# Kernel tuning notes

Measured on AMD Instinct MI355X. Metric: run time of the kernel, lower is better.

The kernel has to match this reference:

```python
import jax, jax.numpy as jnp
import numpy as np
from jax import lax

DN = ('NCHW', 'OIHW', 'NCHW')


def setup_inputs() -> dict:
    key = jax.random.key(0)
    ks = jax.random.split(key, 7)
    B, IC, OC, H, W = 8, 64, 64, 128, 128
    return {
        'x': jax.random.normal(ks[0], (B, IC, H, W), jnp.float32),
        'w3': jax.random.normal(ks[1], (OC, IC, 3, 3), jnp.float32) * 0.05,
        'b3': jax.random.normal(ks[2], (OC,), jnp.float32) * 0.05,
        'w5': jax.random.normal(ks[3], (OC, IC, 5, 5), jnp.float32) * 0.05,
        'b5': jax.random.normal(ks[4], (OC,), jnp.float32) * 0.05,
        'wr': jax.random.normal(ks[5], (OC, 10, 1, 1), jnp.float32) * 0.1,
        'br': jax.random.normal(ks[6], (OC,), jnp.float32) * 0.05,
    }


def reference(x, w3, b3, w5, b5, wr, br):
    # Two 'same' convs (k=3 pad 1, k=5 pad 2) as in layers['5']
    y3 = lax.conv_general_dilated(x, w3, (1, 1), 'SAME', dimension_numbers=DN) + b3[None, :, None, None]
    y5 = lax.conv_general_dilated(x, w5, (1, 1), 'SAME', dimension_numbers=DN) + b5[None, :, None, None]
    B, C, H, W = y3.shape
    # The nested pad/crop loop == 9 zero-padded unit shifts of y3:
    # stackedFeatures order per channel: [y5, shift(sh=0,sw=0..2), shift(sh=1,...), ...]
    # shifted[h, w] = y3[h + 1 - sw, w + 1 - sh] with zero padding.
    P = jnp.pad(y3, ((0, 0), (0, 0), (1, 1), (1, 1)))
    shifts = [P[:, :, 2 - sw:2 - sw + H, 2 - sh:2 - sh + W]
              for sh in range(3) for sw in range(3)]
    stacked = jnp.stack([y5] + shifts, axis=2)  # [B, C, 10, H, W]
    # remap: grouped 1x1 conv, groups=OC, 10 in-channels per group
    out = jnp.einsum('bcghw,cg->bchw', stacked, wr[:, :, 0, 0]) + br[None, :, None, None]
    return out
```

## Files before the change

### kernel.cpp

```cpp
#include <hip/hip_runtime.h>

typedef unsigned short u16;
typedef unsigned int u32;
typedef __attribute__((ext_vector_type(8))) short short8;
typedef __attribute__((ext_vector_type(4))) short short4v;
typedef __attribute__((ext_vector_type(4))) float floatx4;

#define XP 72

__device__ __forceinline__ float bf2f(u16 u) {
    u32 b = ((u32)u) << 16;
    return __builtin_bit_cast(float, b);
}
__device__ __forceinline__ u16 f2bf(float f) {
    u32 b = __builtin_bit_cast(u32, f);
    b += 0x7FFFu + ((b >> 16) & 1u);
    return (u16)(b >> 16);
}

typedef __attribute__((address_space(3))) u16 lds_u16;
typedef const __attribute__((address_space(1))) u16 glob_u16;
__device__ __forceinline__ void gl_lds16(const u16* g, u16* l) {
    __builtin_amdgcn_global_load_lds((glob_u16*)g, (lds_u16*)l, 16, 0, 0);
}

__device__ __forceinline__ float load_any(const void* p, int i, int isf32) {
    return isf32 ? ((const float*)p)[i] : bf2f(((const u16*)p)[i]);
}

__device__ __forceinline__ int sniff_f(const void* x, int* scnt) {
    if (threadIdx.x == 0) *scnt = 0;
    __syncthreads();
    int c = 0;
#pragma unroll
    for (int k = 0; k < 8; ++k) {
        u16 u = ((const u16*)x)[2 * (threadIdx.x * 8 + k)];
        int e = (u >> 7) & 0xFF;
        if (e >= 140) c++;
    }
    if (c) atomicAdd(scnt, c);
    __syncthreads();
    return (*scnt >= 8) ? 1 : 0;
}

#define W5C_BYTE 0
#define SCAL_BYTE 204800
#define V_BYTE 207616
#define XT_BYTE 1272576
#define N_W5C 102400
#define N_SCAL 704
#define PACK_N2 (N_W5C + N_SCAL)

#define VIRT_BLKS 32
#define PACK_BLKS ((PACK_N2 + 255) / 256)
#define TRANS_BLKS 4096

__global__ __launch_bounds__(256) void fuse1(
        const void* __restrict__ x, const void* __restrict__ w3,
        const void* __restrict__ b3, const void* __restrict__ w5,
        const void* __restrict__ b5, const void* __restrict__ wr,
        const void* __restrict__ br,
        u16* __restrict__ w5c, float* __restrict__ scal,
        float* __restrict__ V, u16* __restrict__ xt) {
    __shared__ __align__(16) u16 smem[132 * XP];
    __shared__ int scnt;
    const int bid = blockIdx.x;
    const int tid = threadIdx.x;
    const int f = sniff_f(x, &scnt);

    if (bid < VIRT_BLKS) {
        const int side = bid & 3, b = bid >> 2;
        const int fixed = (side & 1) ? 127 : 0;
        {
            short8 z = {0, 0, 0, 0, 0, 0, 0, 0};
            short8* sp = (short8*)smem;
            for (int i = tid; i < (132 * XP) / 8; i += 256) sp[i] = z;
        }
        __syncthreads();
        {
            const int ic = tid & 63, g = tid >> 6;
            if (side < 2) {
                if (f) {
                    const float* xp = (const float*)x +
                        ((size_t)(b * 64 + ic) * 128 + fixed) * 128;
                    for (int c0 = g * 32; c0 < g * 32 + 32; c0 += 4) {
                        float4 v = *(const float4*)(xp + c0);
                        smem[(c0 + 2) * XP + ic] = f2bf(v.x);
                        smem[(c0 + 3) * XP + ic] = f2bf(v.y);
                        smem[(c0 + 4) * XP + ic] = f2bf(v.z);
                        smem[(c0 + 5) * XP + ic] = f2bf(v.w);
                    }
                } else {
                    const u16* xp = (const u16*)x +
                        ((size_t)(b * 64 + ic) * 128 + fixed) * 128;
                    for (int c0 = g * 32; c0 < g * 32 + 32; c0 += 8) {
                        short8 v = *(const short8*)(xp + c0);
#pragma unroll
                        for (int e = 0; e < 8; ++e)
                            smem[(c0 + 2 + e) * XP + ic] = (u16)v[e];
                    }
                }
            } else {
                if (f) {
                    const float* xp = (const float*)x +
                        (size_t)(b * 64 + ic) * 16384 + fixed;
                    for (int cc = g * 32; cc < g * 32 + 32; ++cc)
                        smem[(cc + 2) * XP + ic] = f2bf(xp[(size_t)cc * 128]);
                } else {
                    const u16* xp = (const u16*)x +
                        (size_t)(b * 64 + ic) * 16384 + fixed;
                    for (int cc = g * 32; cc < g * 32 + 32; ++cc)
                        smem[(cc + 2) * XP + ic] = xp[(size_t)cc * 128];
                }
            }
        }
        const int wv = tid >> 6, lane = tid & 63, cb = lane & 15, q = lane >> 4;
        const int oc = wv * 16 + cb;
        short8 aaA[6];
#pragma unroll
        for (int ks = 0; ks < 6; ++ks) {
            const int kbase = ks * 32 + q * 8;
            const int kk = kbase >> 6, ic0 = kbase & 63;
            int r, c;
            if (side == 0)      { r = 2;  c = kk; }
            else if (side == 1) { r = 0;  c = kk; }
            else if (side == 2) { r = kk; c = 2;  }
            else                { r = kk; c = 0;  }
            short8 a;
#pragma unroll
            for (int j = 0; j < 8; ++j)
                a[j] = (short)f2bf(load_any(w3, (oc * 64 + ic0 + j) * 9 + r * 3 + c, f));
            aaA[ks] = a;
        }
        __syncthreads();

        floatx4 acc[9];
#pragma unroll
        for (int nt = 0; nt < 9; ++nt) acc[nt] = (floatx4){0.f, 0.f, 0.f, 0.f};
#pragma unroll
        for (int ks = 0; ks < 6; ++ks) {
            const int kbase = ks * 32 + q * 8;
            const int kk = kbase >> 6, ic0 = kbase & 63;
#pragma unroll
            for (int nt = 0; nt < 9; ++nt) {
                int p = nt * 16 + cb + kk;
                if (nt == 8 && p > 131) p = 131;
                short8 bb = *(const short8*)&smem[p * XP + ic0];
                acc[nt] = __builtin_amdgcn_mfma_f32_16x16x32_bf16(aaA[ks], bb,
                                                                  acc[nt], 0, 0, 0);
            }
        }
#pragma unroll
        for (int nt = 0; nt < 9; ++nt) {
            int pos = nt * 16 + cb;
            if (pos < 130) {
#pragma unroll
                for (int reg = 0; reg < 4; ++reg) {
                    int oco = wv * 16 + q * 4 + reg;
                    V[((size_t)(b * 4 + side) * 130 + pos) * 64 + oco] =
                        acc[nt][reg] + load_any(b3, oco, f);
                }
            }
        }
        return;
    }

    if (bid < VIRT_BLKS + PACK_BLKS) {
        const int i = (bid - VIRT_BLKS) * 256 + tid;
        if (i >= PACK_N2) return;
        if (i < N_W5C) {
            int j = i & 7, lane = (i >> 3) & 63, mt = (i >> 9) & 3, ks = i >> 11;
            int oc = mt * 16 + (lane & 15);
            int k = ks * 32 + ((lane >> 4) & 3) * 8 + j;
            int tap = k >> 6, ic = k & 63;
            int kh = tap / 5, kw = tap - kh * 5;
            int dh = kh - 2, dw = kw - 2;
            float v = load_any(wr, oc * 10, f) * load_any(w5, (oc * 64 + ic) * 25 + tap, f);
            for (int sw = 0; sw < 3; ++sw) {
                int r = dh + sw;
                if (r < 0 || r > 2) continue;
                for (int sh = 0; sh < 3; ++sh) {
                    int c = dw + sh;
                    if (c < 0 || c > 2) continue;
                    v += load_any(wr, oc * 10 + 1 + sh * 3 + sw, f) *
                         load_any(w3, (oc * 64 + ic) * 9 + r * 3 + c, f);
                }
            }
            w5c[i] = f2bf(v);
        } else {
            int i2 = i - N_W5C;
            float v;
            if (i2 < 64) {
                int oc = i2;
                float swr = 0.f;
                for (int g = 1; g <= 9; ++g) swr += load_any(wr, oc * 10 + g, f);
                v = load_any(wr, oc * 10, f) * load_any(b5, oc, f) +
                    swr * load_any(b3, oc, f) + load_any(br, oc, f);
            } else {
                v = load_any(wr, i2 - 64, f);
            }
            scal[i2] = v;
        }
        return;
    }

    {
        const int t2 = bid - (VIRT_BLKS + PACK_BLKS);
        const int b = t2 >> 9, h = (t2 >> 2) & 127, w0 = (t2 & 3) * 32;
        const int t = tid;
        if (f) {
            const int w2 = t & 15, ic = t >> 4;
#pragma unroll
            for (int p = 0; p < 4; ++p) {
                int icc = ic + p * 16;
                const float* src = (const float*)x +
                    (((size_t)(b * 64 + icc) * 128 + h) * 128 + w0 + 2 * w2);
                float2 v = *(const float2*)src;
                smem[(2 * w2) * XP + icc]     = f2bf(v.x);
                smem[(2 * w2 + 1) * XP + icc] = f2bf(v.y);
            }
        } else {
            const int w4 = t & 7, ic = t >> 3;
#pragma unroll
            for (int p = 0; p < 2; ++p) {
                int icc = ic + p * 32;
                const u16* src = (const u16*)x +
                    (((size_t)(b * 64 + icc) * 128 + h) * 128 + w0 + 4 * w4);
                short4v v = *(const short4v*)src;
#pragma unroll
                for (int e = 0; e < 4; ++e)
                    smem[(4 * w4 + e) * XP + icc] = (u16)v[e];
            }
        }
        __syncthreads();
        const int w = t >> 3, qq = t & 7;
        short8 v = *(const short8*)&smem[w * XP + qq * 8];
        *(short8*)(xt + ((size_t)((b * 128 + h) * 128) + w0 + w) * 64 + qq * 8) = v;
    }
}

__device__ floatx4 edge_fix4(
        const float* __restrict__ Vb, const float* __restrict__ wrf,
        int gh, int gw, int oc0, floatx4 s) {
#pragma unroll
    for (int sh = 0; sh < 3; ++sh)
#pragma unroll
        for (int sw = 0; sw < 3; ++sw) {
            const int qh = gh + 1 - sw, qw = gw + 1 - sh;
            int sd, pos;
            if (qh == -1)       { sd = 0; pos = qw + 1; }
            else if (qh == 128) { sd = 1; pos = qw + 1; }
            else if (qw == -1)  { sd = 2; pos = qh + 1; }
            else if (qw == 128) { sd = 3; pos = qh + 1; }
            else continue;
            const float* vp = Vb + ((size_t)sd * 130 + pos) * 64 + oc0;
            const int wi = 1 + sh * 3 + sw;
#pragma unroll
            for (int r = 0; r < 4; ++r)
                s[r] -= wrf[(oc0 + r) * 10 + wi] * vp[r];
        }
    return s;
}

__global__ __launch_bounds__(256, 2) void conv_fused(
        const void* __restrict__ x,
        const u16* __restrict__ xt, const u16* __restrict__ w5c,
        const float* __restrict__ scal, const float* __restrict__ V,
        void* __restrict__ out) {
    __shared__ __align__(16) u16 xs[400 * XP];
    __shared__ __align__(16) u16 wbuf[2][2][2048];
    __shared__ int scnt;
    const int b = blockIdx.z, h0 = blockIdx.y * 16, w0 = blockIdx.x * 16;
    const int tid = threadIdx.x;
    const int wv = tid >> 6, lane = tid & 63;
    const int f = sniff_f(x, &scnt);

    {
        const int q8 = tid & 7, p0 = tid >> 3;
        for (int it = 0; it < 13; ++it) {
            int px = p0 + it * 32;
            if (px < 400) {
                int r = px / 20, c = px - r * 20;
                int gh = h0 + r - 2, gw = w0 + c - 2;
                short8 v = {0, 0, 0, 0, 0, 0, 0, 0};
                if ((unsigned)gh < 128u && (unsigned)gw < 128u)
                    v = *(const short8*)(xt +
                            ((size_t)((b * 128 + gh) * 128 + gw)) * 64 + q8 * 8);
                *(short8*)&xs[px * XP + q8 * 8] = v;
            }
        }
    }
    gl_lds16(w5c + 0 * 2048 + wv * 512 + lane * 8, &wbuf[0][0][wv * 512]);
    gl_lds16(w5c + 1 * 2048 + wv * 512 + lane * 8, &wbuf[0][1][wv * 512]);
    __syncthreads();

    const int cb = lane & 15, q = lane >> 4, wv4 = wv * 4;
    floatx4 acc[4][4];
#pragma unroll
    for (int mt = 0; mt < 4; ++mt)
#pragma unroll
        for (int nt = 0; nt < 4; ++nt)
            acc[mt][nt] = (floatx4){0.f, 0.f, 0.f, 0.f};

#pragma unroll 1
    for (int tap = 0; tap < 25; ++tap) {
        const int p = tap & 1;
        if (tap + 1 < 25) {
            gl_lds16(w5c + (size_t)((tap + 1) * 2 + 0) * 2048 + wv * 512 + lane * 8,
                     &wbuf[p ^ 1][0][wv * 512]);
            gl_lds16(w5c + (size_t)((tap + 1) * 2 + 1) * 2048 + wv * 512 + lane * 8,
                     &wbuf[p ^ 1][1][wv * 512]);
        }
        const int kh = tap / 5, kw = tap - kh * 5;
#pragma unroll
        for (int s = 0; s < 2; ++s) {
            short8 aa[4], bb[4];
#pragma unroll
            for (int mt = 0; mt < 4; ++mt)
                aa[mt] = *(const short8*)&wbuf[p][s][mt * 512 + lane * 8];
#pragma unroll
            for (int nt = 0; nt < 4; ++nt)
                bb[nt] = *(const short8*)&xs[((wv4 + nt + kh) * 20 + cb + kw) * XP +
                                             s * 32 + q * 8];
#pragma unroll
            for (int nt = 0; nt < 4; ++nt)
#pragma unroll
                for (int mt = 0; mt < 4; ++mt)
                    acc[mt][nt] = __builtin_amdgcn_mfma_f32_16x16x32_bf16(
                        aa[mt], bb[nt], acc[mt][nt], 0, 0, 0);
        }
        __syncthreads();
    }

    const float* biasC = scal;
    const float* wrf = scal + 64;
    const float* Vb = V + (size_t)b * 4 * 130 * 64;
#pragma unroll
    for (int mt = 0; mt < 4; ++mt)
#pragma unroll
        for (int nt = 0; nt < 4; ++nt) {
            const int gh = h0 + wv4 + nt;
            const int gw = w0 + cb;
            const int oc0 = mt * 16 + q * 4;
            floatx4 s;
#pragma unroll
            for (int reg = 0; reg < 4; ++reg)
                s[reg] = acc[mt][nt][reg] + biasC[oc0 + reg];
            if (gh == 0 || gh == 127 || gw == 0 || gw == 127)
                s = edge_fix4(Vb, wrf, gh, gw, oc0, s);
#pragma unroll
            for (int reg = 0; reg < 4; ++reg) {
                size_t oidx = ((size_t)(b * 64 + oc0 + reg) * 128 + gh) * 128 + gw;
                if (f) ((float*)out)[oidx] = s[reg];
                else   ((u16*)out)[oidx]   = f2bf(s[reg]);
            }
        }
}

extern "C" void kernel_launch(void* const* d_in, const int* in_sizes, int n_in,
                              void* d_out, int out_size, void* d_ws, size_t ws_size,
                              hipStream_t stream) {
    const void* x  = d_in[0];
    const void* w3 = d_in[1];
    const void* b3 = d_in[2];
    const void* w5 = d_in[3];
    const void* b5 = d_in[4];
    const void* wr = d_in[5];
    const void* br = d_in[6];

    u16*   w5c  = (u16*)((char*)d_ws + W5C_BYTE);
    float* scal = (float*)((char*)d_ws + SCAL_BYTE);
    float* V    = (float*)((char*)d_ws + V_BYTE);
    u16*   xt   = (u16*)((char*)d_ws + XT_BYTE);

    fuse1<<<VIRT_BLKS + PACK_BLKS + TRANS_BLKS, 256, 0, stream>>>(
        x, w3, b3, w5, b5, wr, br, w5c, scal, V, xt);
    conv_fused<<<dim3(8, 8, 8), 256, 0, stream>>>(x, xt, w5c, scal, V, d_out);
}
```

Before: 166.5 us.

## Split fused prep kernel into sniff, pack/transpose, virtual-edge, and conv launches

Moves the dtype sniff into its own one-block kernel that writes a flag to workspace, so the other blocks read one int instead of each redoing the atomic sniff and its two barriers. The edge-correction (virtual y3 border) MFMA work becomes a separate kernel that reads the already-transposed bf16 xt rather than strided raw x columns. This removes per-block sniff overhead and the uncoalesced column gathers, but adds two extra kernel launches and serialises the edge work after the transpose.

```diff
diff --git a/kernel.cpp b/kernel.cpp
--- a/kernel.cpp
+++ b/kernel.cpp
@@ -28,145 +28,49 @@
     return isf32 ? ((const float*)p)[i] : bf2f(((const u16*)p)[i]);
 }
 
-__device__ __forceinline__ int sniff_f(const void* x, int* scnt) {
-    if (threadIdx.x == 0) *scnt = 0;
-    __syncthreads();
-    int c = 0;
-#pragma unroll
-    for (int k = 0; k < 8; ++k) {
-        u16 u = ((const u16*)x)[2 * (threadIdx.x * 8 + k)];
-        int e = (u >> 7) & 0xFF;
-        if (e >= 140) c++;
-    }
-    if (c) atomicAdd(scnt, c);
-    __syncthreads();
-    return (*scnt >= 8) ? 1 : 0;
-}
-
-#define W5C_BYTE 0
-#define SCAL_BYTE 204800
-#define V_BYTE 207616
-#define XT_BYTE 1272576
+#define FLAG_BYTE 0
+#define W5C_BYTE 256
+#define SCAL_BYTE 205056
+#define V_BYTE 207872
+#define XT_BYTE 1272832
 #define N_W5C 102400
 #define N_SCAL 704
 #define PACK_N2 (N_W5C + N_SCAL)
 
-#define VIRT_BLKS 32
 #define PACK_BLKS ((PACK_N2 + 255) / 256)
 #define TRANS_BLKS 4096
 
-__global__ __launch_bounds__(256) void fuse1(
+__global__ __launch_bounds__(256) void sniff_kernel(const u16* __restrict__ xu,
+                                                    int* __restrict__ flag) {
+    __shared__ int cnt;
+    if (threadIdx.x == 0) cnt = 0;
+    __syncthreads();
+    int c = 0;
+    for (int k = 0; k < 8; ++k) {
+        int idx = 2 * (threadIdx.x * 8 + k);
+        u16 u = xu[idx];
+        int e = (u >> 7) & 0xFF;
+        if (e >= 140) c++;
+    }
+    atomicAdd(&cnt, c);
+    __syncthreads();
+    if (threadIdx.x == 0) *flag = (cnt >= 8) ? 1 : 0;
+}
+
+__global__ __launch_bounds__(256) void pack_trans(
         const void* __restrict__ x, const void* __restrict__ w3,
         const void* __restrict__ b3, const void* __restrict__ w5,
         const void* __restrict__ b5, const void* __restrict__ wr,
-        const void* __restrict__ br,
+        const void* __restrict__ br, const int* __restrict__ flag,
         u16* __restrict__ w5c, float* __restrict__ scal,
-        float* __restrict__ V, u16* __restrict__ xt) {
-    __shared__ __align__(16) u16 smem[132 * XP];
-    __shared__ int scnt;
+        u16* __restrict__ xt) {
+    __shared__ u16 tbuf[32 * XP];
     const int bid = blockIdx.x;
     const int tid = threadIdx.x;
-    const int f = sniff_f(x, &scnt);
-
-    if (bid < VIRT_BLKS) {
-        const int side = bid & 3, b = bid >> 2;
-        const int fixed = (side & 1) ? 127 : 0;
-        {
-            short8 z = {0, 0, 0, 0, 0, 0, 0, 0};
-            short8* sp = (short8*)smem;
-            for (int i = tid; i < (132 * XP) / 8; i += 256) sp[i] = z;
-        }
-        __syncthreads();
-        {
-            const int ic = tid & 63, g = tid >> 6;
-            if (side < 2) {
-                if (f) {
-                    const float* xp = (const float*)x +
-                        ((size_t)(b * 64 + ic) * 128 + fixed) * 128;
-                    for (int c0 = g * 32; c0 < g * 32 + 32; c0 += 4) {
-                        float4 v = *(const float4*)(xp + c0);
-                        smem[(c0 + 2) * XP + ic] = f2bf(v.x);
-                        smem[(c0 + 3) * XP + ic] = f2bf(v.y);
-                        smem[(c0 + 4) * XP + ic] = f2bf(v.z);
-                        smem[(c0 + 5) * XP + ic] = f2bf(v.w);
-                    }
-                } else {
-                    const u16* xp = (const u16*)x +
-                        ((size_t)(b * 64 + ic) * 128 + fixed) * 128;
-                    for (int c0 = g * 32; c0 < g * 32 + 32; c0 += 8) {
-                        short8 v = *(const short8*)(xp + c0);
-#pragma unroll
-                        for (int e = 0; e < 8; ++e)
-                            smem[(c0 + 2 + e) * XP + ic] = (u16)v[e];
-                    }
-                }
-            } else {
-                if (f) {
-                    const float* xp = (const float*)x +
-                        (size_t)(b * 64 + ic) * 16384 + fixed;
-                    for (int cc = g * 32; cc < g * 32 + 32; ++cc)
-                        smem[(cc + 2) * XP + ic] = f2bf(xp[(size_t)cc * 128]);
-                } else {
-                    const u16* xp = (const u16*)x +
-                        (size_t)(b * 64 + ic) * 16384 + fixed;
-                    for (int cc = g * 32; cc < g * 32 + 32; ++cc)
-                        smem[(cc + 2) * XP + ic] = xp[(size_t)cc * 128];
-                }
-            }
-        }
-        const int wv = tid >> 6, lane = tid & 63, cb = lane & 15, q = lane >> 4;
-        const int oc = wv * 16 + cb;
-        short8 aaA[6];
-#pragma unroll
-        for (int ks = 0; ks < 6; ++ks) {
-            const int kbase = ks * 32 + q * 8;
-            const int kk = kbase >> 6, ic0 = kbase & 63;
-            int r, c;
-            if (side == 0)      { r = 2;  c = kk; }
-            else if (side == 1) { r = 0;  c = kk; }
-            else if (side == 2) { r = kk; c = 2;  }
-            else                { r = kk; c = 0;  }
-            short8 a;
-#pragma unroll
-            for (int j = 0; j < 8; ++j)
-                a[j] = (short)f2bf(load_any(w3, (oc * 64 + ic0 + j) * 9 + r * 3 + c, f));
-            aaA[ks] = a;
-        }
-        __syncthreads();
-
-        floatx4 acc[9];
-#pragma unroll
-        for (int nt = 0; nt < 9; ++nt) acc[nt] = (floatx4){0.f, 0.f, 0.f, 0.f};
-#pragma unroll
-        for (int ks = 0; ks < 6; ++ks) {
-            const int kbase = ks * 32 + q * 8;
-            const int kk = kbase >> 6, ic0 = kbase & 63;
-#pragma unroll
-            for (int nt = 0; nt < 9; ++nt) {
-                int p = nt * 16 + cb + kk;
-                if (nt == 8 && p > 131) p = 131;
-                short8 bb = *(const short8*)&smem[p * XP + ic0];
-                acc[nt] = __builtin_amdgcn_mfma_f32_16x16x32_bf16(aaA[ks], bb,
-                                                                  acc[nt], 0, 0, 0);
-            }
-        }
-#pragma unroll
-        for (int nt = 0; nt < 9; ++nt) {
-            int pos = nt * 16 + cb;
-            if (pos < 130) {
-#pragma unroll
-                for (int reg = 0; reg < 4; ++reg) {
-                    int oco = wv * 16 + q * 4 + reg;
-                    V[((size_t)(b * 4 + side) * 130 + pos) * 64 + oco] =
-                        acc[nt][reg] + load_any(b3, oco, f);
-                }
-            }
-        }
-        return;
-    }
-
-    if (bid < VIRT_BLKS + PACK_BLKS) {
-        const int i = (bid - VIRT_BLKS) * 256 + tid;
+    const int f = *flag;
+
+    if (bid < PACK_BLKS) {
+        const int i = bid * 256 + tid;
         if (i >= PACK_N2) return;
         if (i < N_W5C) {
             int j = i & 7, lane = (i >> 3) & 63, mt = (i >> 9) & 3, ks = i >> 11;
@@ -205,7 +109,7 @@
     }
 
     {
-        const int t2 = bid - (VIRT_BLKS + PACK_BLKS);
+        const int t2 = bid - PACK_BLKS;
         const int b = t2 >> 9, h = (t2 >> 2) & 127, w0 = (t2 & 3) * 32;
         const int t = tid;
         if (f) {
@@ -216,8 +120,8 @@
                 const float* src = (const float*)x +
                     (((size_t)(b * 64 + icc) * 128 + h) * 128 + w0 + 2 * w2);
                 float2 v = *(const float2*)src;
-                smem[(2 * w2) * XP + icc]     = f2bf(v.x);
-                smem[(2 * w2 + 1) * XP + icc] = f2bf(v.y);
+                tbuf[(2 * w2) * XP + icc]     = f2bf(v.x);
+                tbuf[(2 * w2 + 1) * XP + icc] = f2bf(v.y);
             }
         } else {
             const int w4 = t & 7, ic = t >> 3;
@@ -229,13 +133,90 @@
                 short4v v = *(const short4v*)src;
 #pragma unroll
                 for (int e = 0; e < 4; ++e)
-                    smem[(4 * w4 + e) * XP + icc] = (u16)v[e];
+                    tbuf[(4 * w4 + e) * XP + icc] = (u16)v[e];
             }
         }
         __syncthreads();
         const int w = t >> 3, qq = t & 7;
-        short8 v = *(const short8*)&smem[w * XP + qq * 8];
+        short8 v = *(const short8*)&tbuf[w * XP + qq * 8];
         *(short8*)(xt + ((size_t)((b * 128 + h) * 128) + w0 + w) * 64 + qq * 8) = v;
+    }
+}
+
+__global__ __launch_bounds__(256) void virt_y3_mfma(
+        const u16* __restrict__ xt, const void* __restrict__ w3,
+        const void* __restrict__ b3, const int* __restrict__ flag,
+        float* __restrict__ V) {
+    __shared__ __align__(16) u16 xrow[132 * XP];
+    const int side = blockIdx.x, b = blockIdx.y;
+    const int tid = threadIdx.x;
+    const int f = *flag;
+    const int fixed = (side & 1) ? 127 : 0;
+    {
+        const int q8 = tid & 7, p0 = tid >> 3;
+#pragma unroll
+        for (int it = 0; it < 5; ++it) {
+            int p = p0 + it * 32;
+            if (p < 132) {
+                int cc = p - 2;
+                short8 v = {0, 0, 0, 0, 0, 0, 0, 0};
+                if ((unsigned)cc < 128u) {
+                    size_t idx = (side < 2)
+                        ? ((size_t)(b * 128 + fixed) * 128 + cc)
+                        : ((size_t)(b * 128 + cc) * 128 + fixed);
+                    v = *(const short8*)(xt + idx * 64 + q8 * 8);
+                }
+                *(short8*)&xrow[p * XP + q8 * 8] = v;
+            }
+        }
+    }
+    const int wv = tid >> 6, lane = tid & 63, cb = lane & 15, q = lane >> 4;
+    const int oc = wv * 16 + cb;
+    short8 aaA[6];
+#pragma unroll
+    for (int ks = 0; ks < 6; ++ks) {
+        const int kbase = ks * 32 + q * 8;
+        const int kk = kbase >> 6, ic0 = kbase & 63;
+        int r, c;
+        if (side == 0)      { r = 2;  c = kk; }
+        else if (side == 1) { r = 0;  c = kk; }
+        else if (side == 2) { r = kk; c = 2;  }
+        else                { r = kk; c = 0;  }
+        short8 a;
+#pragma unroll
+        for (int j = 0; j < 8; ++j)
+            a[j] = (short)f2bf(load_any(w3, (oc * 64 + ic0 + j) * 9 + r * 3 + c, f));
+        aaA[ks] = a;
+    }
+    __syncthreads();
+
+    floatx4 acc[9];
+#pragma unroll
+    for (int nt = 0; nt < 9; ++nt) acc[nt] = (floatx4){0.f, 0.f, 0.f, 0.f};
+#pragma unroll
+    for (int ks = 0; ks < 6; ++ks) {
+        const int kbase = ks * 32 + q * 8;
+        const int kk = kbase >> 6, ic0 = kbase & 63;
+#pragma unroll
+        for (int nt = 0; nt < 9; ++nt) {
+            int p = nt * 16 + cb + kk;
+            if (nt == 8 && p > 131) p = 131;
+            short8 bb = *(const short8*)&xrow[p * XP + ic0];
+            acc[nt] = __builtin_amdgcn_mfma_f32_16x16x32_bf16(aaA[ks], bb,
+                                                              acc[nt], 0, 0, 0);
+        }
+    }
+#pragma unroll
+    for (int nt = 0; nt < 9; ++nt) {
+        int pos = nt * 16 + cb;
+        if (pos < 130) {
+#pragma unroll
+            for (int reg = 0; reg < 4; ++reg) {
+                int oco = wv * 16 + q * 4 + reg;
+                V[((size_t)(b * 4 + side) * 130 + pos) * 64 + oco] =
+                    acc[nt][reg] + load_any(b3, oco, f);
+            }
+        }
     }
 }
 
@@ -262,18 +243,16 @@
     return s;
 }
 
-__global__ __launch_bounds__(256, 2) void conv_fused(
-        const void* __restrict__ x,
+__global__ __launch_bounds__(256, 2) void conv_main(
         const u16* __restrict__ xt, const u16* __restrict__ w5c,
         const float* __restrict__ scal, const float* __restrict__ V,
-        void* __restrict__ out) {
+        const int* __restrict__ flag, void* __restrict__ out) {
     __shared__ __align__(16) u16 xs[400 * XP];
     __shared__ __align__(16) u16 wbuf[2][2][2048];
-    __shared__ int scnt;
     const int b = blockIdx.z, h0 = blockIdx.y * 16, w0 = blockIdx.x * 16;
     const int tid = threadIdx.x;
+    const int f = *flag;
     const int wv = tid >> 6, lane = tid & 63;
-    const int f = sniff_f(x, &scnt);
 
     {
         const int q8 = tid & 7, p0 = tid >> 3;
@@ -368,12 +347,15 @@
     const void* wr = d_in[5];
     const void* br = d_in[6];
 
+    int*   flag = (int*)((char*)d_ws + FLAG_BYTE);
     u16*   w5c  = (u16*)((char*)d_ws + W5C_BYTE);
     float* scal = (float*)((char*)d_ws + SCAL_BYTE);
     float* V    = (float*)((char*)d_ws + V_BYTE);
     u16*   xt   = (u16*)((char*)d_ws + XT_BYTE);
 
-    fuse1<<<VIRT_BLKS + PACK_BLKS + TRANS_BLKS, 256, 0, stream>>>(
-        x, w3, b3, w5, b5, wr, br, w5c, scal, V, xt);
-    conv_fused<<<dim3(8, 8, 8), 256, 0, stream>>>(x, xt, w5c, scal, V, d_out);
-}
+    sniff_kernel<<<1, 256, 0, stream>>>((const u16*)x, flag);
+    pack_trans<<<PACK_BLKS + TRANS_BLKS, 256, 0, stream>>>(
+        x, w3, b3, w5, b5, wr, br, flag, w5c, scal, xt);
+    virt_y3_mfma<<<dim3(4, 8), 256, 0, stream>>>(xt, w3, b3, flag, V);
+    conv_main<<<dim3(8, 8, 8), 256, 0, stream>>>(xt, w5c, scal, V, flag, d_out);
+}
```

After: 161.0 us. 3.3% less time.
